# Optimization experiments

Hardware: AMD Instinct MI355X
Metric: run time of the kernel (lower is better)

The kernel has to match this reference:

```python
import jax, jax.numpy as jnp
import numpy as np
from jax import lax

B, T, N, CIN, CH, COUT, K, KS, E = 2, 16, 2048, 32, 64, 64, 3, 3, 32768


def setup_inputs() -> dict:
    key = jax.random.key(0)
    ks = jax.random.split(key, 20)
    s = 0.05
    p = lambda k, shp: s * jax.random.normal(k, shp, dtype=jnp.float32)
    return {
        "X": jax.random.normal(ks[0], (B, T, N, CIN), dtype=jnp.float32),
        "edge_index": jax.random.randint(ks[1], (2, E), 0, N),
        "edge_weight": jax.random.uniform(ks[2], (E,), dtype=jnp.float32),
        "tc1_w1": p(ks[3], (CH, CIN, 1, KS)), "tc1_b1": p(ks[4], (CH,)),
        "tc1_w2": p(ks[5], (CH, CIN, 1, KS)), "tc1_b2": p(ks[6], (CH,)),
        "tc1_w3": p(ks[7], (CH, CIN, 1, KS)), "tc1_b3": p(ks[8], (CH,)),
        "cheb_w": p(ks[9], (K, CH, CH)), "cheb_b": p(ks[10], (CH,)),
        "tc2_w1": p(ks[11], (COUT, CH, 1, KS)), "tc2_b1": p(ks[12], (COUT,)),
        "tc2_w2": p(ks[13], (COUT, CH, 1, KS)), "tc2_b2": p(ks[14], (COUT,)),
        "tc2_w3": p(ks[15], (COUT, CH, 1, KS)), "tc2_b3": p(ks[16], (COUT,)),
        "bn_gamma": jnp.ones((N,), jnp.float32),
        "bn_beta": jnp.zeros((N,), jnp.float32),
    }


def _tconv(X, w1, b1, w2, b2, w3, b3):
    # X: (B, T, N, C) -> (B, C, N, T), gated temporal conv over last axis
    x = jnp.transpose(X, (0, 3, 2, 1))
    dn = ("NCHW", "OIHW", "NCHW")
    c = lambda w, b: lax.conv_general_dilated(x, w, (1, 1), "VALID", dimension_numbers=dn) + b[None, :, None, None]
    out = jax.nn.relu(c(w1, b1) + jax.nn.sigmoid(c(w2, b2)) + c(w3, b3))
    return jnp.transpose(out, (0, 3, 2, 1))


def _cheb(x, edge_index, edge_weight, W, b):
    # ChebConv, sym normalization, lambda_max=2 -> L_hat = -D^{-1/2} A D^{-1/2}
    row, col = edge_index[0], edge_index[1]
    w = jnp.where(row == col, 0.0, edge_weight)  # get_laplacian removes self-loops
    deg = jax.ops.segment_sum(w, row, num_segments=N)
    safe = jnp.where(deg > 0, deg, 1.0)
    dis = jnp.where(deg > 0, lax.rsqrt(safe), 0.0)
    norm = -dis[row] * w * dis[col]  # (E,)

    def prop(z):  # z: (B, T, N, C)
        zm = jnp.moveaxis(z, 2, 0)                      # (N, B, T, C)
        msg = zm[col] * norm[:, None, None, None]       # (E, B, T, C)
        agg = jax.ops.segment_sum(msg, row, num_segments=N)
        return jnp.moveaxis(agg, 0, 2)

    Tx0 = x
    out = jnp.einsum("btnc,co->btno", Tx0, W[0])
    Tx1 = prop(Tx0)
    out = out + jnp.einsum("btnc,co->btno", Tx1, W[1])
    for k in range(2, K):
        Tx2 = 2.0 * prop(Tx1) - Tx0
        out = out + jnp.einsum("btnc,co->btno", Tx2, W[k])
        Tx0, Tx1 = Tx1, Tx2
    return out + b


def reference(X, edge_index, edge_weight, tc1_w1, tc1_b1, tc1_w2, tc1_b2, tc1_w3, tc1_b3,
              cheb_w, cheb_b, tc2_w1, tc2_b1, tc2_w2, tc2_b2, tc2_w3, tc2_b3,
              bn_gamma, bn_beta):
    t1 = _tconv(X, tc1_w1, tc1_b1, tc1_w2, tc1_b2, tc1_w3, tc1_b3)   # (B, T-2, N, CH)
    t2 = jax.nn.relu(_cheb(t1, edge_index, edge_weight, cheb_w, cheb_b))
    t3 = _tconv(t2, tc2_w1, tc2_b1, tc2_w2, tc2_b2, tc2_w3, tc2_b3)  # (B, T-4, N, COUT)
    t = jnp.transpose(t3, (0, 2, 1, 3))  # (B, N, T', COUT): N is BN channel axis
    mu = jnp.mean(t, axis=(0, 2, 3), keepdims=True)
    var = jnp.var(t, axis=(0, 2, 3), keepdims=True)
    t = (t - mu) * lax.rsqrt(var + 1e-5) * bn_gamma[None, :, None, None] + bn_beta[None, :, None, None]
    return jnp.transpose(t, (0, 2, 1, 3))
```

## Files before the change

### kernel.cpp

```cpp
#include <hip/hip_runtime.h>
#include <cstdint>
#include <cstddef>

typedef unsigned short ushort_t;
typedef short bf16x8 __attribute__((ext_vector_type(8)));
typedef unsigned short u16x8 __attribute__((ext_vector_type(8)));
typedef float f32x4 __attribute__((ext_vector_type(4)));

#define N_NODES 2048
#define E_EDGES 32768
#define BKT_CAP 64

constexpr int SMALL_TOTAL = 72128;
constexpr int OFS_T1B1 = 6144;
constexpr int OFS_T1B2 = 12352;
constexpr int OFS_T1B3 = 18560;
constexpr int OFS_CHB  = 30912;
constexpr int OFS_T2B1 = 43264;
constexpr int OFS_T2B2 = 55616;
constexpr int OFS_T2B3 = 67968;
constexpr int OFS_GAM  = 68032;
constexpr int OFS_BET  = 70080;

__device__ __align__(16) ushort_t g_t1b [3670016];
__device__ __align__(16) ushort_t g_tx1b[3670016];
__device__ float    g_deg[N_NODES];
__device__ int      g_cnt[N_NODES];
__device__ int      g_cur[N_NODES];
__device__ __align__(8) int2 g_bkt[N_NODES * BKT_CAP];
__device__ __align__(16) ushort_t g_can[SMALL_TOTAL];
__device__ __align__(16) ushort_t g_wb1[18432];
__device__ __align__(16) ushort_t g_wb2[36864];
__device__ __align__(16) ushort_t g_wbc[12288];

__device__ __forceinline__ float bfu(ushort_t u) { return __uint_as_float(((unsigned)u) << 16); }
__device__ __forceinline__ ushort_t f2bf(float f) {
    unsigned u = __float_as_uint(f);
    u = u + 0x7fffu + ((u >> 16) & 1u);
    return (ushort_t)(u >> 16);
}
__device__ __forceinline__ float ldin(const void* p, int i, bool isbf) {
    return isbf ? bfu(((const ushort_t*)p)[i]) : ((const float*)p)[i];
}
#define BF16_ONES_PAIR 0x3F803F80u

struct SmallPtrs { const void* p[16]; };
struct WPtrs { const void* p[7]; };

__global__ __launch_bounds__(256) void setup_kernel(const int* __restrict__ ei,
                                                    const void* __restrict__ ew,
                                                    SmallPtrs sp, WPtrs wp,
                                                    const unsigned* __restrict__ gam) {
    const bool isbf = (gam[0] == BF16_ONES_PAIR);
    const int blk = blockIdx.x;
    const int tid = threadIdx.x;
    if (blk < 128) {
        int e = blk * 256 + tid;
        int r = ei[e];
        int c = ei[E_EDGES + e];
        float w = (r == c) ? 0.f : ldin(ew, e, isbf);
        atomicAdd(&g_deg[r], w);
        atomicAdd(&g_cnt[r], 1);
        return;
    }
    if (blk < 410) {
        const int sizes[16] = {6144, 64, 6144, 64, 6144, 64, 12288, 64,
                               12288, 64, 12288, 64, 12288, 64, 2048, 2048};
        int idx = (blk - 128) * 256 + tid;
        if (idx >= SMALL_TOTAL) return;
        int j = 0, local = idx;
        while (local >= sizes[j]) { local -= sizes[j]; ++j; }
        g_can[idx] = isbf ? ((const ushort_t*)sp.p[j])[local]
                          : f2bf(((const float*)sp.p[j])[local]);
        return;
    }
    int idx = (blk - 410) * 256 + tid;
    if (idx < 18432) {
        int j = idx & 7, lane = (idx >> 3) & 63, kk = (idx >> 9) % 3;
        int nt = (idx / 1536) & 3, set = idx / 6144;
        int o = nt * 16 + (lane & 15);
        int k = kk * 32 + (lane >> 4) * 8 + j;
        int ci = k & 31, ks = k >> 5;
        g_wb1[idx] = f2bf(ldin(wp.p[set], o * 96 + ci * 3 + ks, isbf));
    } else if (idx < 18432 + 36864) {
        int t = idx - 18432;
        int j = t & 7, lane = (t >> 3) & 63, kk = (t >> 9) % 6;
        int nt = (t / 3072) & 3, set = t / 12288;
        int o = nt * 16 + (lane & 15);
        int k = kk * 32 + (lane >> 4) * 8 + j;
        int ci = k & 63, ks = k >> 6;
        g_wb2[t] = f2bf(ldin(wp.p[3 + set], o * 192 + ci * 3 + ks, isbf));
    } else {
        int t = idx - 18432 - 36864;
        int j = t & 7, lane = (t >> 3) & 63, kk = (t >> 9) % 6;
        int nt = t / 3072;
        int o = nt * 16 + (lane & 15);
        int k = kk * 32 + (lane >> 4) * 8 + j;
        int sec = k >> 6, c = k & 63;
        g_wbc[t] = f2bf(ldin(wp.p[6], sec * 4096 + c * 64 + o, isbf));
    }
}

__global__ __launch_bounds__(256) void tconv1_mfma_kernel(const void* __restrict__ Xraw,
                                                          const int* __restrict__ ei,
                                                          const void* __restrict__ ew,
                                                          const unsigned* __restrict__ gam) {
    constexpr int T_in  = 16;
    constexpr int T_out = 14;
    constexpr int KST   = 3;
    constexpr int PADK  = 104;

    const bool isbf = (gam[0] == BF16_ONES_PAIR);

    if (blockIdx.x >= 896) {
        int e = (blockIdx.x - 896) * 256 + threadIdx.x;
        int r = ei[e];
        int c = ei[E_EDGES + e];
        float w = (r == c) ? 0.f : ldin(ew, e, isbf);
        float dr = g_deg[r], dc = g_deg[c];
        float nr = dr > 0.f ? rsqrtf(dr) : 0.f;
        float nc = dc > 0.f ? rsqrtf(dc) : 0.f;
        int pos = atomicAdd(&g_cur[r], 1);
        g_bkt[(r << 6) + pos] = make_int2(c, __float_as_int(-nr * w * nc));
        return;
    }

    __shared__ __align__(16) ushort_t xs[64 * PADK];

    const int tid = threadIdx.x;
    const int lane = tid & 63;
    const int wv = tid >> 6;
    const int m0 = blockIdx.x * 64;
    const int n0 = m0 & (N_NODES - 1);
    const int s  = m0 >> 11;
    const int b  = s / T_out;
    const int t  = s - b * T_out;

#pragma unroll
    for (int ks = 0; ks < 3; ++ks) {
        const size_t elo = ((size_t)(b * T_in + t + ks) * N_NODES + n0) * 32;
        if (isbf) {
            const ushort4* src = (const ushort4*)((const ushort_t*)Xraw + elo);
            for (int i = tid; i < 512; i += 256) {
                ushort4 v = src[i];
                int row = i >> 3, c4 = i & 7;
                *(ushort4*)&xs[row * PADK + ks * 32 + c4 * 4] = v;
            }
        } else {
            const float4* src = (const float4*)((const float*)Xraw + elo);
            for (int i = tid; i < 512; i += 256) {
                float4 f = src[i];
                ushort4 v;
                v.x = f2bf(f.x); v.y = f2bf(f.y); v.z = f2bf(f.z); v.w = f2bf(f.w);
                int row = i >> 3, c4 = i & 7;
                *(ushort4*)&xs[row * PADK + ks * 32 + c4 * 4] = v;
            }
        }
    }
    __syncthreads();

    f32x4 acc[3][4];
#pragma unroll
    for (int st = 0; st < 3; ++st)
#pragma unroll
        for (int nt = 0; nt < 4; ++nt) acc[st][nt] = (f32x4){0.f, 0.f, 0.f, 0.f};

    const int arow = wv * 16 + (lane & 15);
    const int kofs = (lane >> 4) * 8;
#pragma unroll
    for (int kk = 0; kk < KST; ++kk) {
        bf16x8 av = *(const bf16x8*)&xs[arow * PADK + kk * 32 + kofs];
#pragma unroll
        for (int st = 0; st < 3; ++st)
#pragma unroll
            for (int nt = 0; nt < 4; ++nt) {
                bf16x8 bv = ((const bf16x8*)g_wb1)[((st * 4 + nt) * KST + kk) * 64 + lane];
                acc[st][nt] = __builtin_amdgcn_mfma_f32_16x16x32_bf16(av, bv, acc[st][nt], 0, 0, 0);
            }
    }

    const int col = lane & 15;
    const int quad = lane >> 4;
#pragma unroll
    for (int nt = 0; nt < 4; ++nt) {
        int o = nt * 16 + col;
        float b1 = bfu(g_can[OFS_T1B1 + o]);
        float b2 = bfu(g_can[OFS_T1B2 + o]);
        float b3 = bfu(g_can[OFS_T1B3 + o]);
#pragma unroll
        for (int reg = 0; reg < 4; ++reg) {
            int m = m0 + wv * 16 + quad * 4 + reg;
            float q = acc[1][nt][reg] + b2;
            float v = (acc[0][nt][reg] + b1) + 1.f / (1.f + expf(-q)) + (acc[2][nt][reg] + b3);
            v = v > 0.f ? v : 0.f;
            g_t1b[(size_t)m * 64 + o] = f2bf(v);
        }
    }
}

__global__ __launch_bounds__(256) void prop0_kernel() {
    const int n = blockIdx.x;
    const int tid = threadIdx.x;
    const int slice = tid >> 3;
    const int ch8   = (tid & 7) * 8;
    if (slice >= 28) return;

    const int beg = n << 6;
    const int end = beg + g_cnt[n];
    const size_t soff = (size_t)slice * (N_NODES * 64) + ch8;

    float a[8];
#pragma unroll
    for (int k = 0; k < 8; ++k) a[k] = 0.f;

    int e = beg;
    for (; e + 4 <= end; e += 4) {
        int2 p0 = g_bkt[e];
        int2 p1 = g_bkt[e + 1];
        int2 p2 = g_bkt[e + 2];
        int2 p3 = g_bkt[e + 3];
        float w0 = __int_as_float(p0.y);
        float w1 = __int_as_float(p1.y);
        float w2 = __int_as_float(p2.y);
        float w3 = __int_as_float(p3.y);
        u16x8 v0 = *(const u16x8*)&g_t1b[soff + ((size_t)p0.x << 6)];
        u16x8 v1 = *(const u16x8*)&g_t1b[soff + ((size_t)p1.x << 6)];
        u16x8 v2 = *(const u16x8*)&g_t1b[soff + ((size_t)p2.x << 6)];
        u16x8 v3 = *(const u16x8*)&g_t1b[soff + ((size_t)p3.x << 6)];
#pragma unroll
        for (int k = 0; k < 8; ++k)
            a[k] = fmaf(w0, bfu(v0[k]), fmaf(w1, bfu(v1[k]),
                   fmaf(w2, bfu(v2[k]), fmaf(w3, bfu(v3[k]), a[k]))));
    }
    for (; e < end; ++e) {
        int2 p = g_bkt[e];
        float w = __int_as_float(p.y);
        u16x8 v = *(const u16x8*)&g_t1b[soff + ((size_t)p.x << 6)];
#pragma unroll
        for (int k = 0; k < 8; ++k) a[k] = fmaf(w, bfu(v[k]), a[k]);
    }

    const size_t o = soff + ((size_t)n << 6);
    u16x8 r;
#pragma unroll
    for (int k = 0; k < 8; ++k) r[k] = f2bf(a[k]);
    *(u16x8*)&g_tx1b[o] = r;
}

__global__ __launch_bounds__(256) void fused_tail_kernel(void* __restrict__ outp,
                                                         const unsigned* __restrict__ gam) {
    __shared__ __align__(16) ushort_t xs[32 * 200];
    __shared__ __align__(16) ushort_t t2s[28 * 72];
    __shared__ float r1[256], r2[256];
    __shared__ float sc_s, sh_s;

    const int n = blockIdx.x;
    const int tid = threadIdx.x;
    const int slice = tid >> 3;
    const int ch8   = (tid & 7) * 8;

    if (slice < 28) {
        const int beg = n << 6;
        const int end = beg + g_cnt[n];
        const size_t soff = (size_t)slice * (N_NODES * 64) + ch8;

        float a[8];
#pragma unroll
        for (int k = 0; k < 8; ++k) a[k] = 0.f;

        int e = beg;
        for (; e + 4 <= end; e += 4) {
            int2 p0 = g_bkt[e];
            int2 p1 = g_bkt[e + 1];
            int2 p2 = g_bkt[e + 2];
            int2 p3 = g_bkt[e + 3];
            float w0 = __int_as_float(p0.y);
            float w1 = __int_as_float(p1.y);
            float w2 = __int_as_float(p2.y);
            float w3 = __int_as_float(p3.y);
            u16x8 v0 = *(const u16x8*)&g_tx1b[soff + ((size_t)p0.x << 6)];
            u16x8 v1 = *(const u16x8*)&g_tx1b[soff + ((size_t)p1.x << 6)];
            u16x8 v2 = *(const u16x8*)&g_tx1b[soff + ((size_t)p2.x << 6)];
            u16x8 v3 = *(const u16x8*)&g_tx1b[soff + ((size_t)p3.x << 6)];
#pragma unroll
            for (int k = 0; k < 8; ++k)
                a[k] = fmaf(w0, bfu(v0[k]), fmaf(w1, bfu(v1[k]),
                       fmaf(w2, bfu(v2[k]), fmaf(w3, bfu(v3[k]), a[k]))));
        }
        for (; e < end; ++e) {
            int2 p = g_bkt[e];
            float w = __int_as_float(p.y);
            u16x8 v = *(const u16x8*)&g_tx1b[soff + ((size_t)p.x << 6)];
#pragma unroll
            for (int k = 0; k < 8; ++k) a[k] = fmaf(w, bfu(v[k]), a[k]);
        }

        const size_t o = soff + ((size_t)n << 6);
        u16x8 t0 = *(const u16x8*)&g_t1b[o];
        u16x8 t1 = *(const u16x8*)&g_tx1b[o];
        u16x8 t2;
#pragma unroll
        for (int k = 0; k < 8; ++k) t2[k] = f2bf(2.f * a[k] - bfu(t0[k]));

        *(u16x8*)&xs[slice * 200 + ch8]        = t0;
        *(u16x8*)&xs[slice * 200 + 64 + ch8]   = t1;
        *(u16x8*)&xs[slice * 200 + 128 + ch8]  = t2;
    } else {
        int r = 28 + ((tid - 224) >> 3);
        u16x8 z = {0, 0, 0, 0, 0, 0, 0, 0};
        *(u16x8*)&xs[r * 200 + ch8]       = z;
        *(u16x8*)&xs[r * 200 + 64 + ch8]  = z;
        *(u16x8*)&xs[r * 200 + 128 + ch8] = z;
    }
    __syncthreads();

    const int lane = tid & 63;
    const int wv = tid >> 6;
    const int mt = wv >> 1;
    const int ntb = (wv & 1) * 2;
    const int col = lane & 15;
    const int quad = lane >> 4;
    const int arow = mt * 16 + col;
    const int kofs = quad * 8;

    {
        f32x4 accb[2];
        accb[0] = (f32x4){0.f, 0.f, 0.f, 0.f};
        accb[1] = (f32x4){0.f, 0.f, 0.f, 0.f};
#pragma unroll
        for (int kk = 0; kk < 6; ++kk) {
            bf16x8 av = *(const bf16x8*)&xs[arow * 200 + kk * 32 + kofs];
#pragma unroll
            for (int i = 0; i < 2; ++i) {
                bf16x8 bv = ((const bf16x8*)g_wbc)[((ntb + i) * 6 + kk) * 64 + lane];
                accb[i] = __builtin_amdgcn_mfma_f32_16x16x32_bf16(av, bv, accb[i], 0, 0, 0);
            }
        }
#pragma unroll
        for (int i = 0; i < 2; ++i) {
            int o = (ntb + i) * 16 + col;
            float bias = bfu(g_can[OFS_CHB + o]);
#pragma unroll
            for (int reg = 0; reg < 4; ++reg) {
                int s = mt * 16 + quad * 4 + reg;
                if (s < 28) {
                    float v = accb[i][reg] + bias;
                    t2s[s * 72 + o] = f2bf(v > 0.f ? v : 0.f);
                }
            }
        }
    }
    __syncthreads();

    const int m_a = arow;
    const int bb  = (m_a >= 12) ? 1 : 0;
    const int rbase = (m_a < 24) ? (m_a + 2 * bb) : 0;

    f32x4 acc2[3][2];
#pragma unroll
    for (int st = 0; st < 3; ++st)
#pragma unroll
        for (int i = 0; i < 2; ++i) acc2[st][i] = (f32x4){0.f, 0.f, 0.f, 0.f};

#pragma unroll
    for (int kk = 0; kk < 6; ++kk) {
        const int ks = kk >> 1;
        const int ci0 = (kk & 1) * 32;
        bf16x8 av = *(const bf16x8*)&t2s[(rbase + ks) * 72 + ci0 + kofs];
#pragma unroll
        for (int st = 0; st < 3; ++st)
#pragma unroll
            for (int i = 0; i < 2; ++i) {
                bf16x8 bv = ((const bf16x8*)g_wb2)[((st * 4 + ntb + i) * 6 + kk) * 64 + lane];
                acc2[st][i] = __builtin_amdgcn_mfma_f32_16x16x32_bf16(av, bv, acc2[st][i], 0, 0, 0);
            }
    }

    float y[2][4];
    float s1 = 0.f, s2 = 0.f;
#pragma unroll
    for (int i = 0; i < 2; ++i) {
        int o = (ntb + i) * 16 + col;
        float b1 = bfu(g_can[OFS_T2B1 + o]);
        float b2 = bfu(g_can[OFS_T2B2 + o]);
        float b3 = bfu(g_can[OFS_T2B3 + o]);
#pragma unroll
        for (int reg = 0; reg < 4; ++reg) {
            int mm = mt * 16 + quad * 4 + reg;
            float q = acc2[1][i][reg] + b2;
            float v = (acc2[0][i][reg] + b1) + 1.f / (1.f + expf(-q)) + (acc2[2][i][reg] + b3);
            v = v > 0.f ? v : 0.f;
            y[i][reg] = v;
            if (mm < 24) { s1 += v; s2 += v * v; }
        }
    }

    r1[tid] = s1;
    r2[tid] = s2;
    __syncthreads();
    for (int st = 128; st > 0; st >>= 1) {
        if (tid < st) { r1[tid] += r1[tid + st]; r2[tid] += r2[tid + st]; }
        __syncthreads();
    }
    if (tid == 0) {
        const float inv = 1.f / 1536.f;
        float mean = r1[0] * inv;
        float var  = r2[0] * inv - mean * mean;
        float rstd = rsqrtf(var + 1e-5f);
        float gm = bfu(g_can[OFS_GAM + n]), be = bfu(g_can[OFS_BET + n]);
        sc_s = rstd * gm;
        sh_s = be - mean * rstd * gm;
    }
    __syncthreads();
    const float sc = sc_s, sh = sh_s;
    const bool isbf = (gam[0] == BF16_ONES_PAIR);

#pragma unroll
    for (int i = 0; i < 2; ++i) {
        int o = (ntb + i) * 16 + col;
#pragma unroll
        for (int reg = 0; reg < 4; ++reg) {
            int mm = mt * 16 + quad * 4 + reg;
            if (mm < 24) {
                size_t off = ((size_t)mm * N_NODES + n) * 64 + o;
                float yy = y[i][reg] * sc + sh;
                if (isbf) ((ushort_t*)outp)[off] = f2bf(yy);
                else      ((float*)outp)[off] = yy;
            }
        }
    }

    if (tid == 0) { g_deg[n] = 0.f; g_cnt[n] = 0; g_cur[n] = 0; }
}

extern "C" void kernel_launch(void* const* d_in, const int* in_sizes, int n_in,
                              void* d_out, int out_size, void* d_ws, size_t ws_size,
                              hipStream_t stream) {
    const void* X = d_in[0];
    const int* ei = (const int*)d_in[1];
    const void* ew = d_in[2];
    const unsigned* gam = (const unsigned*)d_in[17];

    SmallPtrs sp;
    for (int i = 0; i < 16; ++i) sp.p[i] = d_in[3 + i];
    WPtrs wp;
    wp.p[0] = d_in[3];  wp.p[1] = d_in[5];  wp.p[2] = d_in[7];
    wp.p[3] = d_in[11]; wp.p[4] = d_in[13]; wp.p[5] = d_in[15];
    wp.p[6] = d_in[9];

    setup_kernel<<<674, 256, 0, stream>>>(ei, ew, sp, wp, gam);
    tconv1_mfma_kernel<<<1024, 256, 0, stream>>>(X, ei, ew, gam);
    prop0_kernel<<<N_NODES, 256, 0, stream>>>();
    fused_tail_kernel<<<N_NODES, 256, 0, stream>>>(d_out, gam);
}
```

Before: 171.9 us.

## Split fused tail kernel into prop+cheb and tconv2+batchnorm kernels

Splits the fused tail kernel in two. The first kernel does the second propagation plus the Chebyshev MFMA and writes relu output to a new global bf16 buffer. The second kernel reloads that buffer and runs temporal conv 2 and batch norm. This lowers per-kernel LDS and register pressure, which may raise occupancy, but adds a global round trip of about 7 MB and an extra launch.

```diff
diff --git a/kernel.cpp b/kernel.cpp
--- a/kernel.cpp
+++ b/kernel.cpp
@@ -24,6 +24,7 @@
 
 __device__ __align__(16) ushort_t g_t1b [3670016];
 __device__ __align__(16) ushort_t g_tx1b[3670016];
+__device__ __align__(16) ushort_t g_t2b [3670016];
 __device__ float    g_deg[N_NODES];
 __device__ int      g_cnt[N_NODES];
 __device__ int      g_cur[N_NODES];
@@ -247,12 +248,8 @@
     *(u16x8*)&g_tx1b[o] = r;
 }
 
-__global__ __launch_bounds__(256) void fused_tail_kernel(void* __restrict__ outp,
-                                                         const unsigned* __restrict__ gam) {
+__global__ __launch_bounds__(256) void prop_cheb_kernel() {
     __shared__ __align__(16) ushort_t xs[32 * 200];
-    __shared__ __align__(16) ushort_t t2s[28 * 72];
-    __shared__ float r1[256], r2[256];
-    __shared__ float sc_s, sh_s;
 
     const int n = blockIdx.x;
     const int tid = threadIdx.x;
@@ -318,41 +315,64 @@
     const int wv = tid >> 6;
     const int mt = wv >> 1;
     const int ntb = (wv & 1) * 2;
+    const int arow = mt * 16 + (lane & 15);
+    const int kofs = (lane >> 4) * 8;
+
+    f32x4 acc[2];
+    acc[0] = (f32x4){0.f, 0.f, 0.f, 0.f};
+    acc[1] = (f32x4){0.f, 0.f, 0.f, 0.f};
+#pragma unroll
+    for (int kk = 0; kk < 6; ++kk) {
+        bf16x8 av = *(const bf16x8*)&xs[arow * 200 + kk * 32 + kofs];
+#pragma unroll
+        for (int i = 0; i < 2; ++i) {
+            bf16x8 bv = ((const bf16x8*)g_wbc)[((ntb + i) * 6 + kk) * 64 + lane];
+            acc[i] = __builtin_amdgcn_mfma_f32_16x16x32_bf16(av, bv, acc[i], 0, 0, 0);
+        }
+    }
+
     const int col = lane & 15;
     const int quad = lane >> 4;
-    const int arow = mt * 16 + col;
+#pragma unroll
+    for (int i = 0; i < 2; ++i) {
+        int o = (ntb + i) * 16 + col;
+        float bias = bfu(g_can[OFS_CHB + o]);
+#pragma unroll
+        for (int reg = 0; reg < 4; ++reg) {
+            int m = mt * 16 + quad * 4 + reg;
+            if (m < 28) {
+                float v = acc[i][reg] + bias;
+                g_t2b[((size_t)(m * N_NODES + n)) * 64 + o] = f2bf(v > 0.f ? v : 0.f);
+            }
+        }
+    }
+}
+
+__global__ __launch_bounds__(256) void tconv2bn_kernel(void* __restrict__ outp,
+                                                       const unsigned* __restrict__ gam) {
+    __shared__ __align__(16) ushort_t t2s[28 * 72];
+    __shared__ float r1[256], r2[256];
+    __shared__ float sc_s, sh_s;
+
+    const int n = blockIdx.x;
+    const int tid = threadIdx.x;
+
+    if (tid < 224) {
+        int row = tid >> 3, c8 = (tid & 7) * 8;
+        u16x8 v = *(const u16x8*)&g_t2b[((size_t)(row * N_NODES + n)) * 64 + c8];
+        *(u16x8*)&t2s[row * 72 + c8] = v;
+    }
+    __syncthreads();
+
+    const int lane = tid & 63;
+    const int wv = tid >> 6;
+    const int mt = wv >> 1;
+    const int ntb = (wv & 1) * 2;
+    const int col = lane & 15;
+    const int quad = lane >> 4;
     const int kofs = quad * 8;
 
-    {
-        f32x4 accb[2];
-        accb[0] = (f32x4){0.f, 0.f, 0.f, 0.f};
-        accb[1] = (f32x4){0.f, 0.f, 0.f, 0.f};
-#pragma unroll
-        for (int kk = 0; kk < 6; ++kk) {
-            bf16x8 av = *(const bf16x8*)&xs[arow * 200 + kk * 32 + kofs];
-#pragma unroll
-            for (int i = 0; i < 2; ++i) {
-                bf16x8 bv = ((const bf16x8*)g_wbc)[((ntb + i) * 6 + kk) * 64 + lane];
-                accb[i] = __builtin_amdgcn_mfma_f32_16x16x32_bf16(av, bv, accb[i], 0, 0, 0);
-            }
-        }
-#pragma unroll
-        for (int i = 0; i < 2; ++i) {
-            int o = (ntb + i) * 16 + col;
-            float bias = bfu(g_can[OFS_CHB + o]);
-#pragma unroll
-            for (int reg = 0; reg < 4; ++reg) {
-                int s = mt * 16 + quad * 4 + reg;
-                if (s < 28) {
-                    float v = accb[i][reg] + bias;
-                    t2s[s * 72 + o] = f2bf(v > 0.f ? v : 0.f);
-                }
-            }
-        }
-    }
-    __syncthreads();
-
-    const int m_a = arow;
+    const int m_a = mt * 16 + col;
     const int bb  = (m_a >= 12) ? 1 : 0;
     const int rbase = (m_a < 24) ? (m_a + 2 * bb) : 0;
 
@@ -451,5 +471,6 @@
     setup_kernel<<<674, 256, 0, stream>>>(ei, ew, sp, wp, gam);
     tconv1_mfma_kernel<<<1024, 256, 0, stream>>>(X, ei, ew, gam);
     prop0_kernel<<<N_NODES, 256, 0, stream>>>();
-    fused_tail_kernel<<<N_NODES, 256, 0, stream>>>(d_out, gam);
-}
+    prop_cheb_kernel<<<N_NODES, 256, 0, stream>>>();
+    tconv2bn_kernel<<<N_NODES, 256, 0, stream>>>(d_out, gam);
+}
```

Result: slower. 176.6 us (+2.7%).
